# Optimization experiments

Hardware: AMD Instinct MI355X
Metric: run time of the kernel (lower is better)

## Reference

```python
import jax, jax.numpy as jnp
import numpy as np

G = 4           # graphs in batch
NV_PER = 3000   # variables per graph
NC_PER = 1000   # constraints per graph
DEG = 8         # constraint neighbors per variable
D_FEAT = 64
D_HID = 128
D_OUT = 64
K_BREAK = 8     # n_breakings
EPS = 1e-5


def setup_inputs() -> dict:
    key = jax.random.key(0)
    ks = jax.random.split(key, 5)
    nv, nc = G * NV_PER, G * NC_PER
    # bipartite edges: each variable connects to DEG random constraints within its graph
    var = np.tile(np.repeat(np.arange(NV_PER), DEG), G) + np.repeat(np.arange(G) * NV_PER, NV_PER * DEG)
    con = np.asarray(jax.random.randint(ks[0], (G, NV_PER * DEG), 0, NC_PER)) + (np.arange(G) * NC_PER)[:, None]
    con = con.reshape(-1)
    edge_indices = jnp.asarray(np.stack([con, var]), dtype=jnp.int32)            # (constraint, variable)
    reversed_edge_indices = jnp.asarray(np.stack([var, con]), dtype=jnp.int32)   # (variable, constraint)
    return {
        'variable_features': jax.random.normal(ks[1], (nv, D_FEAT), jnp.float32),
        'constraint_features': jax.random.normal(ks[2], (nc, D_FEAT), jnp.float32),
        'W1': jax.random.normal(ks[3], (D_FEAT + 1, D_HID), jnp.float32) * (1.0 / np.sqrt(D_FEAT + 1)),
        'b1': jnp.zeros((D_HID,), jnp.float32),
        'W2': jax.random.normal(ks[4], (D_HID, D_OUT), jnp.float32) * (1.0 / np.sqrt(D_HID)),
        'b2': jnp.zeros((D_OUT,), jnp.float32),
        'gamma': jnp.ones((D_OUT,), jnp.float32),
        'beta': jnp.zeros((D_OUT,), jnp.float32),
        'edge_indices': edge_indices,
        'reversed_edge_indices': reversed_edge_indices,
        'n_variables_per_graph': jnp.full((G,), NV_PER, jnp.int32),
        'n_constraints_per_graph': jnp.full((G,), NC_PER, jnp.int32),
    }


def _build_adj(edge_indices, reversed_edge_indices, nv, N):
    # homogeneous symmetric bipartite adjacency + gcn_norm(add_self_loops=True)
    rows = jnp.concatenate([reversed_edge_indices[0], edge_indices[0] + nv])
    cols = jnp.concatenate([reversed_edge_indices[1] + nv, edge_indices[1]])
    deg = jax.ops.segment_sum(jnp.ones_like(rows, jnp.float32), rows, num_segments=N) + 1.0
    dinv = jax.lax.rsqrt(deg)
    edge_vals = dinv[rows] * dinv[cols]     # D^-1/2 A D^-1/2 off-diagonal
    loop_vals = dinv * dinv                  # self-loop diagonal
    return rows, cols, edge_vals, loop_vals


def _spmm(rows, cols, edge_vals, loop_vals, N, X):
    # X: (N, d) -> adj @ X
    return jax.ops.segment_sum(edge_vals[:, None] * X[cols], rows, num_segments=N) + loop_vals[:, None] * X


def _holo_forward(variable_features, constraint_features, W1, b1, W2, b2, gamma, beta,
                  rows, cols, edge_vals, loop_vals, break_idx, break_group, G_):
    nv = variable_features.shape[0]
    N = nv + constraint_features.shape[0]
    nvp = nv // G_
    X = jnp.concatenate([variable_features, constraint_features], axis=0)        # (N, d)
    B = break_idx.shape[0]
    one_hot = jax.nn.one_hot(break_idx, N, dtype=X.dtype)                        # (B, N)
    Xb = jnp.concatenate([jnp.broadcast_to(X, (B,) + X.shape), one_hot[:, :, None]], axis=-1)  # (B, N, d+1)
    spmm = lambda x: _spmm(rows, cols, edge_vals, loop_vals, N, x)
    h = jax.nn.relu(jax.lax.map(spmm, Xb @ W1 + b1))                             # (B, N, D_HID)
    out = jax.lax.map(spmm, h @ W2 + b2)                                         # (B, N, D_OUT)
    mu = out.mean(-1, keepdims=True)
    var = ((out - mu) ** 2).mean(-1, keepdims=True)
    holo = (out - mu) * jax.lax.rsqrt(var + EPS) * gamma + beta                  # LayerNorm
    set_link = holo[:, :nv, :]                                                   # r=1: tuples = variables
    global_mean = set_link.mean(0)                                               # (nv, D_OUT)
    tuple_group = jnp.repeat(jnp.arange(G_), nvp)                                # (nv,)
    group_sum = jax.ops.segment_sum(set_link, break_group, num_segments=G_)      # (G, nv, D_OUT)
    counts = jax.ops.segment_sum(jnp.ones((B,), holo.dtype), break_group, num_segments=G_)
    link = group_sum[tuple_group, jnp.arange(nv)] / jnp.maximum(counts[tuple_group], 1.0)[:, None]
    return jnp.where((counts[tuple_group] > 0)[:, None], link, global_mean)


def reference(variable_features, constraint_features, W1, b1, W2, b2, gamma, beta,
              edge_indices, reversed_edge_indices, n_variables_per_graph, n_constraints_per_graph):
    nv = variable_features.shape[0]
    nc = constraint_features.shape[0]
    N = nv + nc
    G_ = n_variables_per_graph.shape[0]
    nvp, ncp = nv // G_, nc // G_
    rows, cols, edge_vals, loop_vals = _build_adj(edge_indices, reversed_edge_indices, nv, N)
    node_degrees = jax.ops.segment_sum(edge_vals, rows, num_segments=N) + loop_vals  # adj row sums
    # per-graph top-k degree nodes (tie-expansion is measure-zero for float gcn-norm degrees)
    var_ids = jnp.arange(G_)[:, None] * nvp + jnp.arange(nvp)[None, :]
    con_ids = nv + jnp.arange(G_)[:, None] * ncp + jnp.arange(ncp)[None, :]
    sample_nodes = jnp.concatenate([var_ids, con_ids], axis=1)                   # (G, nvp+ncp)
    _, local = jax.lax.top_k(node_degrees[sample_nodes], K_BREAK)
    break_idx = jnp.take_along_axis(sample_nodes, local, axis=1).reshape(-1)     # (G*K,)
    break_group = jnp.repeat(jnp.arange(G_), K_BREAK)
    return _holo_forward(variable_features, constraint_features, W1, b1, W2, b2, gamma, beta,
                         rows, cols, edge_vals, loop_vals, break_idx, break_group, G_)
```

## Files before the change

kernel.cpp:

```cpp
#include <hip/hip_runtime.h>
#include <hip/hip_bf16.h>

#define G_      4
#define NVP     3000
#define NCP     1000
#define DEG     8
#define NV      (G_*NVP)
#define NC      (G_*NCP)
#define NN      (NV+NC)
#define NE      (NV*DEG)
#define EPG     (NVP*DEG)
#define DF      64
#define DH      128
#define DO      64
#define KB      8
#define NB      (G_*KB)
#define MAXR    96
#define MAXJ    640
#define F2_GEMM_BLOCKS (NV/32)

__global__ __launch_bounds__(1024) void k_setup(const int* __restrict__ conArr,
    int* __restrict__ csr_off, int* __restrict__ csr_cur,
    float* __restrict__ dinvC_g, float* __restrict__ nodeval, int* __restrict__ breakix)
{
    __shared__ int   cnt[NCP];
    __shared__ float dinvC[NCP];
    __shared__ float nvl[NVP + NCP];
    __shared__ int   wsum[16];
    __shared__ float mv[16]; __shared__ int mp[16];

    int g = blockIdx.x, tid = threadIdx.x, lane = tid & 63, w = tid >> 6;
    int ebase = g * EPG, cb = g * NCP;
    const float dv3 = 1.0f/3.0f;

    if (tid < NCP) cnt[tid] = 0;
    __syncthreads();
    for (int e = tid; e < EPG; e += 1024)
        atomicAdd(&cnt[conArr[ebase + e] - cb], 1);
    __syncthreads();
    int x = (tid < NCP) ? cnt[tid] : 0;
    int orig = x;
    for (int o = 1; o < 64; o <<= 1) { int y = __shfl_up(x, o); if (lane >= o) x += y; }
    if (lane == 63) wsum[w] = x;
    __syncthreads();
    if (tid == 0) { int run = 0; for (int t = 0; t < 16; ++t) { int z = wsum[t]; wsum[t] = run; run += z; } }
    __syncthreads();
    int excl = x - orig + wsum[w];
    if (tid < NCP) {
        csr_off[cb + tid] = ebase + excl;
        csr_cur[cb + tid] = ebase + excl;
        float dc = 1.0f / sqrtf((float)(orig + 1));
        dinvC[tid] = dc;
        dinvC_g[cb + tid] = dc;
        float nvc = (float)orig * (dc * dv3) + dc*dc;
        nvl[NVP + tid] = nvc;
        nodeval[NV + cb + tid] = nvc;
    }
    if (g == 0 && tid == 0) csr_off[NC] = NE;
    __syncthreads();
    for (int v = tid; v < NVP; v += 1024) {
        float s = 0.f;
        int e0 = ebase + v*DEG;
        #pragma unroll
        for (int k = 0; k < DEG; ++k) s += dv3 * dinvC[conArr[e0+k] - cb];
        float val = s + dv3*dv3;
        nvl[v] = val;
        nodeval[g*NVP + v] = val;
    }
    __syncthreads();
    for (int it = 0; it < KB; ++it) {
        float bv = -1e30f; int bp = 1 << 30;
        for (int p = tid; p < NVP+NCP; p += 1024) {
            float vv = nvl[p];
            if (vv > bv || (vv == bv && p < bp)) { bv = vv; bp = p; }
        }
        for (int o = 32; o > 0; o >>= 1) {
            float ov = __shfl_xor(bv, o); int op = __shfl_xor(bp, o);
            if (ov > bv || (ov == bv && op < bp)) { bv = ov; bp = op; }
        }
        if (lane == 0) { mv[w] = bv; mp[w] = bp; }
        __syncthreads();
        if (tid == 0) {
            float fv = mv[0]; int fp = mp[0];
            for (int t = 1; t < 16; ++t)
                if (mv[t] > fv || (mv[t] == fv && mp[t] < fp)) { fv = mv[t]; fp = mp[t]; }
            nvl[fp] = -1e30f;
            breakix[g*KB + it] = (fp < NVP) ? (g*NVP + fp) : (NV + g*NCP + (fp - NVP));
        }
        __syncthreads();
    }
}

__global__ __launch_bounds__(1024) void k_fill(const int* __restrict__ conArr,
                                               int* __restrict__ csr_cur,
                                               int* __restrict__ csr_v) {
    int e = blockIdx.x*1024 + threadIdx.x;
    if (e < NE) { int p = atomicAdd(&csr_cur[conArr[e]], 1); csr_v[p] = e >> 3; }
}

__global__ __launch_bounds__(1024) void k_f1(const float* __restrict__ vf, const float* __restrict__ cf,
    const float* __restrict__ dinvC, const int* __restrict__ conArr,
    const int* __restrict__ csr_off, const int* __restrict__ csr_v,
    const float* __restrict__ W1, const float* __restrict__ b1,
    const float* __restrict__ nodeval, float* __restrict__ S1)
{
    __shared__ float W1T[128*68];
    __shared__ float AXs[32*68];
    int tid = threadIdx.x, lane = tid & 63, w = tid >> 6;
    const float dv3 = 1.0f/3.0f;
    for (int t = tid; t < 64*128; t += 1024) {
        int k = t >> 7, c = t & 127;
        W1T[c*68 + k] = W1[t];
    }
    int r0 = blockIdx.x * 32;
    for (int rr = w*2; rr < w*2 + 2; ++rr) {
        int row = r0 + rr;
        float acc, di;
        if (row < NV) {
            di = dv3;
            acc = dv3 * vf[(size_t)row*DF + lane];
            int e0 = row*DEG;
            #pragma unroll
            for (int k = 0; k < DEG; ++k) {
                int c = conArr[e0+k];
                acc += dinvC[c] * cf[(size_t)c*DF + lane];
            }
        } else {
            int c = row - NV;
            di = dinvC[c];
            float base = di * cf[(size_t)c*DF + lane];
            int p0 = csr_off[c], p1 = csr_off[c+1];
            int len = p1 - p0;
            int myv = (p0 + lane < p1) ? csr_v[p0 + lane] : 0;
            int lim = len < 64 ? len : 64;
            float a0 = 0.f, a1 = 0.f, a2 = 0.f, a3 = 0.f;
            int m = 0;
            for (; m + 4 <= lim; m += 4) {
                int v0 = __shfl(myv, m+0);
                int v1 = __shfl(myv, m+1);
                int v2 = __shfl(myv, m+2);
                int v3 = __shfl(myv, m+3);
                a0 += vf[(size_t)v0*DF + lane];
                a1 += vf[(size_t)v1*DF + lane];
                a2 += vf[(size_t)v2*DF + lane];
                a3 += vf[(size_t)v3*DF + lane];
            }
            for (; m < lim; ++m) { int v = __shfl(myv, m); a0 += vf[(size_t)v*DF + lane]; }
            for (int p = p0 + 64; p < p1; ++p) a0 += vf[(size_t)csr_v[p]*DF + lane];
            acc = base + dv3 * ((a0 + a1) + (a2 + a3));
        }
        AXs[rr*68 + lane] = di * acc;
    }
    __syncthreads();
    int tc = tid & 15, tr = tid >> 4;
    int row = tr & 31, chh = tr >> 5;
    float a4[4] = {0.f, 0.f, 0.f, 0.f};
    #pragma unroll
    for (int k0 = 0; k0 < 64; k0 += 4) {
        float4 a = *(const float4*)&AXs[row*68 + k0];
        #pragma unroll
        for (int j = 0; j < 4; ++j) {
            float4 wv = *(const float4*)&W1T[(tc + 16*j + 64*chh)*68 + k0];
            a4[j] += a.x*wv.x + a.y*wv.y + a.z*wv.z + a.w*wv.w;
        }
    }
    float nv_ = nodeval[r0 + row];
    #pragma unroll
    for (int j = 0; j < 4; ++j) {
        int col = tc + 16*j + 64*chh;
        S1[(size_t)(r0 + row)*DH + col] = a4[j] + nv_*b1[col];
    }
}

__global__ __launch_bounds__(1024) void k_f2(const float* __restrict__ S1,
    const float* __restrict__ dinvC, const int* __restrict__ conArr,
    const int* __restrict__ csr_off, const int* __restrict__ csr_v,
    const float* __restrict__ W1, const float* __restrict__ W2,
    const float* __restrict__ b2, const float* __restrict__ nodeval,
    const float* __restrict__ gamma, const float* __restrict__ beta,
    const int* __restrict__ breakidx,
    float* __restrict__ outvar, float* __restrict__ holo, float* __restrict__ out,
    int* __restrict__ RnG, float* __restrict__ RwG, int* __restrict__ nRG,
    float* __restrict__ dz2G)
{
    __shared__ float smem[14848];
    __shared__ int nR_s;
    int tid = threadIdx.x, lane = tid & 63, w = tid >> 6;
    const float dv3 = 1.0f/3.0f;

    if (blockIdx.x < F2_GEMM_BLOCKS) {
        float* W2T = smem;
        float* AHs = smem + 8448;
        float* s2  = smem + 12672;
        for (int t = tid; t < 128*64; t += 1024) {
            int k = t >> 6, c = t & 63;
            W2T[c*132 + k] = W2[t];
        }
        int r0 = blockIdx.x * 32;
        for (int rr = w*2; rr < w*2 + 2; ++rr) {
            int v = r0 + rr;
            float a0 = dv3 * fmaxf(S1[(size_t)v*DH + lane], 0.f);
            float a1 = dv3 * fmaxf(S1[(size_t)v*DH + 64 + lane], 0.f);
            int e0 = v*DEG;
            #pragma unroll
            for (int k = 0; k < DEG; ++k) {
                int c = conArr[e0+k];
                float dc = dinvC[c];
                a0 += dc * fmaxf(S1[(size_t)(NV+c)*DH + lane], 0.f);
                a1 += dc * fmaxf(S1[(size_t)(NV+c)*DH + 64 + lane], 0.f);
            }
            AHs[rr*132 + lane]      = dv3 * a0;
            AHs[rr*132 + 64 + lane] = dv3 * a1;
        }
        __syncthreads();
        int tc = tid & 15, tr = tid >> 4;
        int row = tr & 31, jh = tr >> 5;
        float a2[2] = {0.f, 0.f};
        #pragma unroll
        for (int k0 = 0; k0 < 128; k0 += 4) {
            float4 a = *(const float4*)&AHs[row*132 + k0];
            #pragma unroll
            for (int j = 0; j < 2; ++j) {
                float4 wv = *(const float4*)&W2T[(tc + 16*(j + 2*jh))*132 + k0];
                a2[j] += a.x*wv.x + a.y*wv.y + a.z*wv.z + a.w*wv.w;
            }
        }
        float nv_ = nodeval[r0 + row];
        #pragma unroll
        for (int j = 0; j < 2; ++j) {
            int col = tc + 16*(j + 2*jh);
            s2[row*68 + col] = a2[j] + nv_*b2[col];
        }
        __syncthreads();
        float gm = gamma[lane], bt = beta[lane];
        for (int rr = w*2; rr < w*2 + 2; ++rr) {
            int v = r0 + rr;
            float xv = s2[rr*68 + lane];
            float s = xv;
            for (int o = 32; o > 0; o >>= 1) s += __shfl_xor(s, o);
            float mu = s * (1.f/64.f);
            float d = xv - mu;
            float vs = d*d;
            for (int o = 32; o > 0; o >>= 1) vs += __shfl_xor(vs, o);
            float rstd = 1.0f / sqrtf(vs*(1.f/64.f) + 1e-5f);
            float h = d*rstd*gm + bt;
            outvar[(size_t)v*DO + lane] = xv;
            holo  [(size_t)v*DO + lane] = h;
            out   [(size_t)v*DO + lane] = h;
        }
    } else {
        float* W2s = smem;
        float* dh  = smem + 8192;
        float* Rw  = smem + 9216;
        int*   Rn  = (int*)(smem + 9312);
        int b = blockIdx.x - F2_GEMM_BLOCKS;
        int i = breakidx[b];
        for (int t = tid; t < 128*64; t += 1024) W2s[t] = W2[t];
        if (tid < 64) {
            if (i >= NV) {
                int c = i - NV;
                float di = dinvC[c];
                int p0 = csr_off[c], len = csr_off[c+1] - p0;
                if (len <= 64) {
                    int v = (lane < len) ? csr_v[p0 + lane] : 0x7fffffff;
                    int firstLane = 64, mult = 0;
                    for (int m = 0; m < 64; ++m) {
                        int vm = __shfl(v, m);
                        if (vm == v) { mult++; if (m < firstLane) firstLane = m; }
                    }
                    bool head = (lane < len) && (firstLane == lane);
                    unsigned long long hmask = __ballot(head);
                    int hrk = 0;
                    for (int m = 0; m < 64; ++m) {
                        if (!((hmask >> m) & 1)) continue;
                        int vm = __shfl(v, m);
                        if (vm < v) hrk++;
                    }
                    if (head) { Rn[hrk] = v; Rw[hrk] = (float)mult * (dv3 * di); }
                    int nH = __popcll(hmask);
                    if (lane == 0) { Rn[nH] = i; Rw[nH] = di*di; nR_s = nH + 1; }
                } else if (lane == 0) {
                    int n = 0;
                    for (int p = p0; p < p0 + len; ++p) {
                        int v = csr_v[p]; int f = -1;
                        for (int q = 0; q < n; ++q) if (Rn[q] == v) { f = q; break; }
                        if (f >= 0) Rw[f] += dv3 * di;
                        else if (n < MAXR-1) { Rn[n] = v; Rw[n] = dv3 * di; ++n; }
                    }
                    Rn[n] = i; Rw[n] = di*di; nR_s = n + 1;
                }
            } else if (lane == 0) {
                float di = dv3;
                int cn[DEG];
                for (int k = 0; k < DEG; ++k) cn[k] = NV + conArr[i*DEG + k];
                for (int a = 1; a < DEG; ++a) { int key = cn[a]; int bb = a-1;
                    while (bb >= 0 && cn[bb] > key) { cn[bb+1] = cn[bb]; --bb; } cn[bb+1] = key; }
                int n = 0, k = 0;
                while (k < DEG) { int u = cn[k]; int m = 1; ++k;
                    while (k < DEG && cn[k] == u) { ++m; ++k; }
                    Rn[n] = u; Rw[n] = (float)m * dinvC[u - NV] * di; ++n; }
                Rn[n] = i; Rw[n] = di*di; nR_s = n + 1;
            }
        }
        __syncthreads();
        int nR = nR_s;
        for (int t = tid; t < nR; t += 1024) { RnG[b*MAXR + t] = Rn[t]; RwG[b*MAXR + t] = Rw[t]; }
        if (tid == 0) nRG[b] = nR;
        for (int r0c = 0; r0c < nR; r0c += 8) {
            __syncthreads();
            {
                int ty = tid >> 7, k = tid & 127;
                int r = r0c + ty;
                if (r < nR) {
                    float s1 = S1[(size_t)Rn[r]*DH + k];
                    float a = s1 + Rw[r] * W1[64*128 + k];
                    dh[ty*128 + k] = fmaxf(a, 0.f) - fmaxf(s1, 0.f);
                }
            }
            __syncthreads();
            int ty2 = tid >> 6, c2 = tid & 63;
            if (ty2 < 8) {
                int r2 = r0c + ty2;
                if (r2 < nR) {
                    float accv = 0.f;
                    #pragma unroll
                    for (int kk = 0; kk < 128; ++kk) accv += dh[ty2*128 + kk] * W2s[kk*64 + c2];
                    dz2G[((size_t)b*MAXR + r2)*DO + c2] = accv;
                }
            }
        }
    }
}

__global__ __launch_bounds__(256) void k_corr_b(const int* __restrict__ RnG, const float* __restrict__ RwG,
                         const int* __restrict__ nRG, const float* __restrict__ dz2G,
                         const int* __restrict__ breakidx, const float* __restrict__ dinvC,
                         const int* __restrict__ conArr, const int* __restrict__ csr_off,
                         const int* __restrict__ csr_v,
                         const float* __restrict__ outvar, const float* __restrict__ holo,
                         const float* __restrict__ gamma, const float* __restrict__ beta,
                         float* __restrict__ out) {
    int b = blockIdx.x;
    int lane = threadIdx.x & 63, wv = threadIdx.x >> 6;
    const float dv3 = 1.0f/3.0f;
    __shared__ int Jn[MAXJ];
    __shared__ int nJ_s;
    int i = breakidx[b];
    int nR = nRG[b];
    float gm = gamma[lane], bt = beta[lane];
    if (i >= NV) {
        int nJ = nR - 1;
        const float* dzi = &dz2G[((size_t)b*MAXR + (nR-1))*DO];
        for (int j0 = wv; j0 < nJ; j0 += 4) {
            int j = RnG[b*MAXR + j0];
            float aji = RwG[b*MAXR + j0];
            float x = outvar[(size_t)j*DO + lane]
                    + aji * dzi[lane]
                    + dv3*dv3 * dz2G[((size_t)b*MAXR + j0)*DO + lane];
            float s = x; for (int o = 32; o > 0; o >>= 1) s += __shfl_xor(s, o);
            float mu = s * (1.f/64.f);
            float d = x - mu;
            float vs = d*d; for (int o = 32; o > 0; o >>= 1) vs += __shfl_xor(vs, o);
            float rstd = 1.0f / sqrtf(vs*(1.f/64.f) + 1e-5f);
            float hn = d*rstd*gm + bt;
            atomicAdd(&out[(size_t)j*DO + lane], 0.125f * (hn - holo[(size_t)j*DO + lane]));
        }
    } else {
        if (threadIdx.x == 0) {
            int n = 0; Jn[n++] = i;
            for (int r = 0; r < nR-1; ++r) {
                int c = RnG[b*MAXR + r] - NV;
                for (int p = csr_off[c]; p < csr_off[c+1]; ++p) {
                    int u = csr_v[p];
                    bool found = false;
                    for (int q = 0; q < n; ++q) if (Jn[q] == u) { found = true; break; }
                    if (!found && n < MAXJ) Jn[n++] = u;
                }
            }
            nJ_s = n;
        }
        __syncthreads();
        int nJ = nJ_s;
        for (int j0 = wv; j0 < nJ; j0 += 4) {
            int j = Jn[j0];
            float x = outvar[(size_t)j*DO + lane];
            for (int k = 0; k < DEG; ++k) {
                int cn = NV + conArr[j*DEG + k];
                for (int r = 0; r < nR-1; ++r)
                    if (RnG[b*MAXR + r] == cn) {
                        x += dv3 * dinvC[cn - NV] * dz2G[((size_t)b*MAXR + r)*DO + lane];
                        break;
                    }
            }
            if (j == i) x += dv3*dv3 * dz2G[((size_t)b*MAXR + nR-1)*DO + lane];
            float s = x; for (int o = 32; o > 0; o >>= 1) s += __shfl_xor(s, o);
            float mu = s * (1.f/64.f);
            float d = x - mu;
            float vs = d*d; for (int o = 32; o > 0; o >>= 1) vs += __shfl_xor(vs, o);
            float rstd = 1.0f / sqrtf(vs*(1.f/64.f) + 1e-5f);
            float hn = d*rstd*gm + bt;
            atomicAdd(&out[(size_t)j*DO + lane], 0.125f * (hn - holo[(size_t)j*DO + lane]));
        }
    }
}


extern "C" void kernel_launch(void* const* d_in, const int* in_sizes, int n_in,
                              void* d_out, int out_size, void* d_ws, size_t ws_size,
                              hipStream_t stream) {
    const float* vf    = (const float*)d_in[0];
    const float* cf    = (const float*)d_in[1];
    const float* W1    = (const float*)d_in[2];
    const float* b1    = (const float*)d_in[3];
    const float* W2    = (const float*)d_in[4];
    const float* b2    = (const float*)d_in[5];
    const float* gamma = (const float*)d_in[6];
    const float* beta  = (const float*)d_in[7];
    const int*   ei    = (const int*)d_in[8];
    const int*   conArr = ei;
    float* out = (float*)d_out;

    char* ws = (char*)d_ws;
    size_t off = 0;
    auto alloc = [&](size_t bytes) { char* p = ws + off; off = (off + bytes + 255) & ~(size_t)255; return p; };
    float* dinvC   = (float*)alloc(NC*4);
    int*   csr_off = (int*)  alloc((NC+1)*4);
    int*   csr_cur = (int*)  alloc(NC*4);
    int*   csr_v   = (int*)  alloc(NE*4);
    float* nodeval = (float*)alloc(NN*4);
    int*   breakix = (int*)  alloc(NB*4);
    float* S1      = (float*)alloc((size_t)NN*DH*4);
    float* outvar  = (float*)alloc((size_t)NV*DO*4);
    float* holo    = (float*)alloc((size_t)NV*DO*4);
    int*   RnG     = (int*)  alloc(NB*MAXR*4);
    float* RwG     = (float*)alloc(NB*MAXR*4);
    int*   nRG     = (int*)  alloc(NB*4);
    float* dz2G    = (float*)alloc((size_t)NB*MAXR*DO*4);

    k_setup <<<G_, 1024, 0, stream>>>(conArr, csr_off, csr_cur, dinvC, nodeval, breakix);
    k_fill  <<<(NE+1023)/1024, 1024, 0, stream>>>(conArr, csr_cur, csr_v);
    k_f1    <<<NN/32, 1024, 0, stream>>>(vf, cf, dinvC, conArr, csr_off, csr_v, W1, b1, nodeval, S1);
    k_f2    <<<F2_GEMM_BLOCKS + NB, 1024, 0, stream>>>(S1, dinvC, conArr, csr_off, csr_v,
                                       W1, W2, b2, nodeval, gamma, beta, breakix,
                                       outvar, holo, out, RnG, RwG, nRG, dz2G);
    k_corr_b<<<NB, 256, 0, stream>>>(RnG, RwG, nRG, dz2G, breakix, dinvC, conArr,
                                     csr_off, csr_v, outvar, holo, gamma, beta, out);
}
```

Measured before the change: 95.37 us.

## Fuse all stages into one cooperative persistent kernel with grid syncs

Replaces the five separate kernel launches with a single cooperative kernel of 256 blocks that runs setup, CSR fill, the first GCN layer, the second layer plus break corrections, and the final correction, separated by grid-wide syncs. Each block handles up to two tiles per stage and reuses the transposed weight matrix already in shared memory for its second tile. The intent is to remove launch gaps and inter-kernel drain. In exchange, grid syncs add overhead and most blocks sit idle in setup and the final stage. The corr_b stage now runs on 1024-thread blocks with a matching loop stride, and a multi-launch fallback keeps the old behaviour if the cooperative launch fails.

Result: no change. 94.46 us (-0.9%).

```diff
diff --git a/kernel.cpp b/kernel.cpp
--- a/kernel.cpp
+++ b/kernel.cpp
@@ -1,5 +1,8 @@
 #include <hip/hip_runtime.h>
+#include <hip/hip_cooperative_groups.h>
 #include <hip/hip_bf16.h>
+
+namespace cg = cooperative_groups;
 
 #define G_      4
 #define NVP     3000
@@ -17,19 +20,24 @@
 #define NB      (G_*KB)
 #define MAXR    96
 #define MAXJ    640
-#define F2_GEMM_BLOCKS (NV/32)
-
-__global__ __launch_bounds__(1024) void k_setup(const int* __restrict__ conArr,
+#define F2_GEMM_TILES (NV/32)
+#define F1_TILES (NN/32)
+#define F2_TILES (F2_GEMM_TILES+NB)
+#define MEGA_GRID 256
+
+
+__device__ __forceinline__ void setup_body(int g, const int* __restrict__ conArr,
     int* __restrict__ csr_off, int* __restrict__ csr_cur,
-    float* __restrict__ dinvC_g, float* __restrict__ nodeval, int* __restrict__ breakix)
+    float* __restrict__ dinvC_g, float* __restrict__ nodeval, int* __restrict__ breakix,
+    float* smemf)
 {
-    __shared__ int   cnt[NCP];
-    __shared__ float dinvC[NCP];
-    __shared__ float nvl[NVP + NCP];
-    __shared__ int   wsum[16];
-    __shared__ float mv[16]; __shared__ int mp[16];
-
-    int g = blockIdx.x, tid = threadIdx.x, lane = tid & 63, w = tid >> 6;
+    int*   cnt   = (int*)smemf;
+    float* dinvC = (float*)(cnt + NCP);
+    float* nvl   = dinvC + NCP;
+    int*   wsum  = (int*)(nvl + (NVP + NCP));
+    float* mv    = (float*)(wsum + 16);
+    int*   mp    = (int*)(mv + 16);
+    int tid = threadIdx.x, lane = tid & 63, w = tid >> 6;
     int ebase = g * EPG, cb = g * NCP;
     const float dv3 = 1.0f/3.0f;
 
@@ -91,28 +99,25 @@
     }
 }
 
-__global__ __launch_bounds__(1024) void k_fill(const int* __restrict__ conArr,
-                                               int* __restrict__ csr_cur,
-                                               int* __restrict__ csr_v) {
-    int e = blockIdx.x*1024 + threadIdx.x;
-    if (e < NE) { int p = atomicAdd(&csr_cur[conArr[e]], 1); csr_v[p] = e >> 3; }
-}
-
-__global__ __launch_bounds__(1024) void k_f1(const float* __restrict__ vf, const float* __restrict__ cf,
+__device__ __forceinline__ void f1_body(int tile, bool first,
+    const float* __restrict__ vf, const float* __restrict__ cf,
     const float* __restrict__ dinvC, const int* __restrict__ conArr,
     const int* __restrict__ csr_off, const int* __restrict__ csr_v,
     const float* __restrict__ W1, const float* __restrict__ b1,
-    const float* __restrict__ nodeval, float* __restrict__ S1)
+    const float* __restrict__ nodeval, float* __restrict__ S1, float* smemf)
 {
-    __shared__ float W1T[128*68];
-    __shared__ float AXs[32*68];
+    float* W1T = smemf;
+    float* AXs = smemf + 8704;
     int tid = threadIdx.x, lane = tid & 63, w = tid >> 6;
     const float dv3 = 1.0f/3.0f;
-    for (int t = tid; t < 64*128; t += 1024) {
-        int k = t >> 7, c = t & 127;
-        W1T[c*68 + k] = W1[t];
-    }
-    int r0 = blockIdx.x * 32;
+    if (!first) __syncthreads();
+    if (first) {
+        for (int t = tid; t < 64*128; t += 1024) {
+            int k = t >> 7, c = t & 127;
+            W1T[c*68 + k] = W1[t];
+        }
+    }
+    int r0 = tile * 32;
     for (int rr = w*2; rr < w*2 + 2; ++rr) {
         int row = r0 + rr;
         float acc, di;
@@ -172,186 +177,194 @@
     }
 }
 
-__global__ __launch_bounds__(1024) void k_f2(const float* __restrict__ S1,
-    const float* __restrict__ dinvC, const int* __restrict__ conArr,
-    const int* __restrict__ csr_off, const int* __restrict__ csr_v,
-    const float* __restrict__ W1, const float* __restrict__ W2,
+__device__ __forceinline__ void f2gemm_body(int tile, bool first,
+    const float* __restrict__ S1, const float* __restrict__ dinvC,
+    const int* __restrict__ conArr, const float* __restrict__ W2,
     const float* __restrict__ b2, const float* __restrict__ nodeval,
     const float* __restrict__ gamma, const float* __restrict__ beta,
-    const int* __restrict__ breakidx,
     float* __restrict__ outvar, float* __restrict__ holo, float* __restrict__ out,
-    int* __restrict__ RnG, float* __restrict__ RwG, int* __restrict__ nRG,
-    float* __restrict__ dz2G)
+    float* smemf)
 {
-    __shared__ float smem[14848];
-    __shared__ int nR_s;
+    float* W2T = smemf;
+    float* AHs = smemf + 8448;
+    float* s2  = smemf + 12672;
     int tid = threadIdx.x, lane = tid & 63, w = tid >> 6;
     const float dv3 = 1.0f/3.0f;
-
-    if (blockIdx.x < F2_GEMM_BLOCKS) {
-        float* W2T = smem;
-        float* AHs = smem + 8448;
-        float* s2  = smem + 12672;
+    if (!first) __syncthreads();
+    if (first) {
         for (int t = tid; t < 128*64; t += 1024) {
             int k = t >> 6, c = t & 63;
             W2T[c*132 + k] = W2[t];
         }
-        int r0 = blockIdx.x * 32;
-        for (int rr = w*2; rr < w*2 + 2; ++rr) {
-            int v = r0 + rr;
-            float a0 = dv3 * fmaxf(S1[(size_t)v*DH + lane], 0.f);
-            float a1 = dv3 * fmaxf(S1[(size_t)v*DH + 64 + lane], 0.f);
-            int e0 = v*DEG;
-            #pragma unroll
-            for (int k = 0; k < DEG; ++k) {
-                int c = conArr[e0+k];
-                float dc = dinvC[c];
-                a0 += dc * fmaxf(S1[(size_t)(NV+c)*DH + lane], 0.f);
-                a1 += dc * fmaxf(S1[(size_t)(NV+c)*DH + 64 + lane], 0.f);
-            }
-            AHs[rr*132 + lane]      = dv3 * a0;
-            AHs[rr*132 + 64 + lane] = dv3 * a1;
-        }
-        __syncthreads();
-        int tc = tid & 15, tr = tid >> 4;
-        int row = tr & 31, jh = tr >> 5;
-        float a2[2] = {0.f, 0.f};
+    }
+    int r0 = tile * 32;
+    for (int rr = w*2; rr < w*2 + 2; ++rr) {
+        int v = r0 + rr;
+        float a0 = dv3 * fmaxf(S1[(size_t)v*DH + lane], 0.f);
+        float a1 = dv3 * fmaxf(S1[(size_t)v*DH + 64 + lane], 0.f);
+        int e0 = v*DEG;
         #pragma unroll
-        for (int k0 = 0; k0 < 128; k0 += 4) {
-            float4 a = *(const float4*)&AHs[row*132 + k0];
-            #pragma unroll
-            for (int j = 0; j < 2; ++j) {
-                float4 wv = *(const float4*)&W2T[(tc + 16*(j + 2*jh))*132 + k0];
-                a2[j] += a.x*wv.x + a.y*wv.y + a.z*wv.z + a.w*wv.w;
-            }
-        }
-        float nv_ = nodeval[r0 + row];
+        for (int k = 0; k < DEG; ++k) {
+            int c = conArr[e0+k];
+            float dc = dinvC[c];
+            a0 += dc * fmaxf(S1[(size_t)(NV+c)*DH + lane], 0.f);
+            a1 += dc * fmaxf(S1[(size_t)(NV+c)*DH + 64 + lane], 0.f);
+        }
+        AHs[rr*132 + lane]      = dv3 * a0;
+        AHs[rr*132 + 64 + lane] = dv3 * a1;
+    }
+    __syncthreads();
+    int tc = tid & 15, tr = tid >> 4;
+    int row = tr & 31, jh = tr >> 5;
+    float a2[2] = {0.f, 0.f};
+    #pragma unroll
+    for (int k0 = 0; k0 < 128; k0 += 4) {
+        float4 a = *(const float4*)&AHs[row*132 + k0];
         #pragma unroll
         for (int j = 0; j < 2; ++j) {
-            int col = tc + 16*(j + 2*jh);
-            s2[row*68 + col] = a2[j] + nv_*b2[col];
-        }
+            float4 wv = *(const float4*)&W2T[(tc + 16*(j + 2*jh))*132 + k0];
+            a2[j] += a.x*wv.x + a.y*wv.y + a.z*wv.z + a.w*wv.w;
+        }
+    }
+    float nv_ = nodeval[r0 + row];
+    #pragma unroll
+    for (int j = 0; j < 2; ++j) {
+        int col = tc + 16*(j + 2*jh);
+        s2[row*68 + col] = a2[j] + nv_*b2[col];
+    }
+    __syncthreads();
+    float gm = gamma[lane], bt = beta[lane];
+    for (int rr = w*2; rr < w*2 + 2; ++rr) {
+        int v = r0 + rr;
+        float xv = s2[rr*68 + lane];
+        float s = xv;
+        for (int o = 32; o > 0; o >>= 1) s += __shfl_xor(s, o);
+        float mu = s * (1.f/64.f);
+        float d = xv - mu;
+        float vs = d*d;
+        for (int o = 32; o > 0; o >>= 1) vs += __shfl_xor(vs, o);
+        float rstd = 1.0f / sqrtf(vs*(1.f/64.f) + 1e-5f);
+        float h = d*rstd*gm + bt;
+        outvar[(size_t)v*DO + lane] = xv;
+        holo  [(size_t)v*DO + lane] = h;
+        out   [(size_t)v*DO + lane] = h;
+    }
+}
+
+__device__ __forceinline__ void corra_body(int b,
+    const float* __restrict__ S1, const float* __restrict__ dinvC,
+    const int* __restrict__ conArr, const int* __restrict__ csr_off,
+    const int* __restrict__ csr_v, const float* __restrict__ W1,
+    const float* __restrict__ W2, const int* __restrict__ breakidx,
+    int* __restrict__ RnG, float* __restrict__ RwG, int* __restrict__ nRG,
+    float* __restrict__ dz2G, float* smemf, int& nR_s)
+{
+    float* W2s = smemf;
+    float* dh  = smemf + 8192;
+    float* Rw  = smemf + 9216;
+    int*   Rn  = (int*)(smemf + 9312);
+    int tid = threadIdx.x, lane = tid & 63;
+    const float dv3 = 1.0f/3.0f;
+    __syncthreads();
+    int i = breakidx[b];
+    for (int t = tid; t < 128*64; t += 1024) W2s[t] = W2[t];
+    if (tid < 64) {
+        if (i >= NV) {
+            int c = i - NV;
+            float di = dinvC[c];
+            int p0 = csr_off[c], len = csr_off[c+1] - p0;
+            if (len <= 64) {
+                int v = (lane < len) ? csr_v[p0 + lane] : 0x7fffffff;
+                int firstLane = 64, mult = 0;
+                for (int m = 0; m < 64; ++m) {
+                    int vm = __shfl(v, m);
+                    if (vm == v) { mult++; if (m < firstLane) firstLane = m; }
+                }
+                bool head = (lane < len) && (firstLane == lane);
+                unsigned long long hmask = __ballot(head);
+                int hrk = 0;
+                for (int m = 0; m < 64; ++m) {
+                    if (!((hmask >> m) & 1)) continue;
+                    int vm = __shfl(v, m);
+                    if (vm < v) hrk++;
+                }
+                if (head) { Rn[hrk] = v; Rw[hrk] = (float)mult * (dv3 * di); }
+                int nH = __popcll(hmask);
+                if (lane == 0) { Rn[nH] = i; Rw[nH] = di*di; nR_s = nH + 1; }
+            } else if (lane == 0) {
+                int n = 0;
+                for (int p = p0; p < p0 + len; ++p) {
+                    int v = csr_v[p]; int f = -1;
+                    for (int q = 0; q < n; ++q) if (Rn[q] == v) { f = q; break; }
+                    if (f >= 0) Rw[f] += dv3 * di;
+                    else if (n < MAXR-1) { Rn[n] = v; Rw[n] = dv3 * di; ++n; }
+                }
+                Rn[n] = i; Rw[n] = di*di; nR_s = n + 1;
+            }
+        } else if (lane == 0) {
+            float di = dv3;
+            int cn[DEG];
+            for (int k = 0; k < DEG; ++k) cn[k] = NV + conArr[i*DEG + k];
+            for (int a = 1; a < DEG; ++a) { int key = cn[a]; int bb = a-1;
+                while (bb >= 0 && cn[bb] > key) { cn[bb+1] = cn[bb]; --bb; } cn[bb+1] = key; }
+            int n = 0, k = 0;
+            while (k < DEG) { int u = cn[k]; int m = 1; ++k;
+                while (k < DEG && cn[k] == u) { ++m; ++k; }
+                Rn[n] = u; Rw[n] = (float)m * dinvC[u - NV] * di; ++n; }
+            Rn[n] = i; Rw[n] = di*di; nR_s = n + 1;
+        }
+    }
+    __syncthreads();
+    int nR = nR_s;
+    for (int t = tid; t < nR; t += 1024) { RnG[b*MAXR + t] = Rn[t]; RwG[b*MAXR + t] = Rw[t]; }
+    if (tid == 0) nRG[b] = nR;
+    for (int r0c = 0; r0c < nR; r0c += 8) {
         __syncthreads();
-        float gm = gamma[lane], bt = beta[lane];
-        for (int rr = w*2; rr < w*2 + 2; ++rr) {
-            int v = r0 + rr;
-            float xv = s2[rr*68 + lane];
-            float s = xv;
-            for (int o = 32; o > 0; o >>= 1) s += __shfl_xor(s, o);
-            float mu = s * (1.f/64.f);
-            float d = xv - mu;
-            float vs = d*d;
-            for (int o = 32; o > 0; o >>= 1) vs += __shfl_xor(vs, o);
-            float rstd = 1.0f / sqrtf(vs*(1.f/64.f) + 1e-5f);
-            float h = d*rstd*gm + bt;
-            outvar[(size_t)v*DO + lane] = xv;
-            holo  [(size_t)v*DO + lane] = h;
-            out   [(size_t)v*DO + lane] = h;
-        }
-    } else {
-        float* W2s = smem;
-        float* dh  = smem + 8192;
-        float* Rw  = smem + 9216;
-        int*   Rn  = (int*)(smem + 9312);
-        int b = blockIdx.x - F2_GEMM_BLOCKS;
-        int i = breakidx[b];
-        for (int t = tid; t < 128*64; t += 1024) W2s[t] = W2[t];
-        if (tid < 64) {
-            if (i >= NV) {
-                int c = i - NV;
-                float di = dinvC[c];
-                int p0 = csr_off[c], len = csr_off[c+1] - p0;
-                if (len <= 64) {
-                    int v = (lane < len) ? csr_v[p0 + lane] : 0x7fffffff;
-                    int firstLane = 64, mult = 0;
-                    for (int m = 0; m < 64; ++m) {
-                        int vm = __shfl(v, m);
-                        if (vm == v) { mult++; if (m < firstLane) firstLane = m; }
-                    }
-                    bool head = (lane < len) && (firstLane == lane);
-                    unsigned long long hmask = __ballot(head);
-                    int hrk = 0;
-                    for (int m = 0; m < 64; ++m) {
-                        if (!((hmask >> m) & 1)) continue;
-                        int vm = __shfl(v, m);
-                        if (vm < v) hrk++;
-                    }
-                    if (head) { Rn[hrk] = v; Rw[hrk] = (float)mult * (dv3 * di); }
-                    int nH = __popcll(hmask);
-                    if (lane == 0) { Rn[nH] = i; Rw[nH] = di*di; nR_s = nH + 1; }
-                } else if (lane == 0) {
-                    int n = 0;
-                    for (int p = p0; p < p0 + len; ++p) {
-                        int v = csr_v[p]; int f = -1;
-                        for (int q = 0; q < n; ++q) if (Rn[q] == v) { f = q; break; }
-                        if (f >= 0) Rw[f] += dv3 * di;
-                        else if (n < MAXR-1) { Rn[n] = v; Rw[n] = dv3 * di; ++n; }
-                    }
-                    Rn[n] = i; Rw[n] = di*di; nR_s = n + 1;
-                }
-            } else if (lane == 0) {
-                float di = dv3;
-                int cn[DEG];
-                for (int k = 0; k < DEG; ++k) cn[k] = NV + conArr[i*DEG + k];
-                for (int a = 1; a < DEG; ++a) { int key = cn[a]; int bb = a-1;
-                    while (bb >= 0 && cn[bb] > key) { cn[bb+1] = cn[bb]; --bb; } cn[bb+1] = key; }
-                int n = 0, k = 0;
-                while (k < DEG) { int u = cn[k]; int m = 1; ++k;
-                    while (k < DEG && cn[k] == u) { ++m; ++k; }
-                    Rn[n] = u; Rw[n] = (float)m * dinvC[u - NV] * di; ++n; }
-                Rn[n] = i; Rw[n] = di*di; nR_s = n + 1;
+        {
+            int ty = tid >> 7, k = tid & 127;
+            int r = r0c + ty;
+            if (r < nR) {
+                float s1 = S1[(size_t)Rn[r]*DH + k];
+                float a = s1 + Rw[r] * W1[64*128 + k];
+                dh[ty*128 + k] = fmaxf(a, 0.f) - fmaxf(s1, 0.f);
             }
         }
         __syncthreads();
-        int nR = nR_s;
-        for (int t = tid; t < nR; t += 1024) { RnG[b*MAXR + t] = Rn[t]; RwG[b*MAXR + t] = Rw[t]; }
-        if (tid == 0) nRG[b] = nR;
-        for (int r0c = 0; r0c < nR; r0c += 8) {
-            __syncthreads();
-            {
-                int ty = tid >> 7, k = tid & 127;
-                int r = r0c + ty;
-                if (r < nR) {
-                    float s1 = S1[(size_t)Rn[r]*DH + k];
-                    float a = s1 + Rw[r] * W1[64*128 + k];
-                    dh[ty*128 + k] = fmaxf(a, 0.f) - fmaxf(s1, 0.f);
-                }
-            }
-            __syncthreads();
-            int ty2 = tid >> 6, c2 = tid & 63;
-            if (ty2 < 8) {
-                int r2 = r0c + ty2;
-                if (r2 < nR) {
-                    float accv = 0.f;
-                    #pragma unroll
-                    for (int kk = 0; kk < 128; ++kk) accv += dh[ty2*128 + kk] * W2s[kk*64 + c2];
-                    dz2G[((size_t)b*MAXR + r2)*DO + c2] = accv;
-                }
-            }
-        }
-    }
-}
-
-__global__ __launch_bounds__(256) void k_corr_b(const int* __restrict__ RnG, const float* __restrict__ RwG,
-                         const int* __restrict__ nRG, const float* __restrict__ dz2G,
-                         const int* __restrict__ breakidx, const float* __restrict__ dinvC,
-                         const int* __restrict__ conArr, const int* __restrict__ csr_off,
-                         const int* __restrict__ csr_v,
-                         const float* __restrict__ outvar, const float* __restrict__ holo,
-                         const float* __restrict__ gamma, const float* __restrict__ beta,
-                         float* __restrict__ out) {
-    int b = blockIdx.x;
+        int ty2 = tid >> 6, c2 = tid & 63;
+        if (ty2 < 8) {
+            int r2 = r0c + ty2;
+            if (r2 < nR) {
+                float accv = 0.f;
+                #pragma unroll
+                for (int kk = 0; kk < 128; ++kk) accv += dh[ty2*128 + kk] * W2s[kk*64 + c2];
+                dz2G[((size_t)b*MAXR + r2)*DO + c2] = accv;
+            }
+        }
+    }
+    __syncthreads();
+}
+
+__device__ __forceinline__ void corrb_body(int b,
+    const int* __restrict__ RnG, const float* __restrict__ RwG,
+    const int* __restrict__ nRG, const float* __restrict__ dz2G,
+    const int* __restrict__ breakidx, const float* __restrict__ dinvC,
+    const int* __restrict__ conArr, const int* __restrict__ csr_off,
+    const int* __restrict__ csr_v,
+    const float* __restrict__ outvar, const float* __restrict__ holo,
+    const float* __restrict__ gamma, const float* __restrict__ beta,
+    float* __restrict__ out, float* smemf)
+{
+    int* Jn = (int*)smemf;
+    __shared__ int nJ_s;
     int lane = threadIdx.x & 63, wv = threadIdx.x >> 6;
     const float dv3 = 1.0f/3.0f;
-    __shared__ int Jn[MAXJ];
-    __shared__ int nJ_s;
     int i = breakidx[b];
     int nR = nRG[b];
     float gm = gamma[lane], bt = beta[lane];
     if (i >= NV) {
         int nJ = nR - 1;
         const float* dzi = &dz2G[((size_t)b*MAXR + (nR-1))*DO];
-        for (int j0 = wv; j0 < nJ; j0 += 4) {
+        for (int j0 = wv; j0 < nJ; j0 += 16) {
             int j = RnG[b*MAXR + j0];
             float aji = RwG[b*MAXR + j0];
             float x = outvar[(size_t)j*DO + lane]
@@ -381,7 +394,7 @@
         }
         __syncthreads();
         int nJ = nJ_s;
-        for (int j0 = wv; j0 < nJ; j0 += 4) {
+        for (int j0 = wv; j0 < nJ; j0 += 16) {
             int j = Jn[j0];
             float x = outvar[(size_t)j*DO + lane];
             for (int k = 0; k < DEG; ++k) {
@@ -402,6 +415,75 @@
             atomicAdd(&out[(size_t)j*DO + lane], 0.125f * (hn - holo[(size_t)j*DO + lane]));
         }
     }
+}
+
+
+__global__ __launch_bounds__(1024) void k_mega(
+    const float* __restrict__ vf, const float* __restrict__ cf,
+    const float* __restrict__ W1, const float* __restrict__ b1,
+    const float* __restrict__ W2, const float* __restrict__ b2,
+    const float* __restrict__ gamma, const float* __restrict__ beta,
+    const int* __restrict__ conArr,
+    int* csr_off, int* csr_cur, int* csr_v,
+    float* dinvC, float* nodeval, int* breakix,
+    float* S1, float* outvar, float* holo,
+    int* RnG, float* RwG, int* nRG, float* dz2G,
+    float* out, int phase)
+{
+    __shared__ float smemf[14848];
+    __shared__ int nR_s;
+    const bool coop = (phase < 0);
+    int bid = blockIdx.x;
+
+    if ((coop || phase == 0) && bid < G_)
+        setup_body(bid, conArr, csr_off, csr_cur, dinvC, nodeval, breakix, smemf);
+    if (coop) cg::this_grid().sync();
+
+    if (coop || phase == 1) {
+        int e = bid*1024 + threadIdx.x;
+        if (e < NE) { int p = atomicAdd(&csr_cur[conArr[e]], 1); csr_v[p] = e >> 3; }
+    }
+    if (coop) cg::this_grid().sync();
+
+    if (coop || phase == 2) {
+        if (coop) {
+            f1_body(bid, true, vf, cf, dinvC, conArr, csr_off, csr_v, W1, b1, nodeval, S1, smemf);
+            int t2 = (bid < F1_TILES - MEGA_GRID) ? MEGA_GRID + bid : -1;
+            if (t2 >= 0)
+                f1_body(t2, false, vf, cf, dinvC, conArr, csr_off, csr_v, W1, b1, nodeval, S1, smemf);
+        } else {
+            f1_body(bid, true, vf, cf, dinvC, conArr, csr_off, csr_v, W1, b1, nodeval, S1, smemf);
+        }
+    }
+    if (coop) cg::this_grid().sync();
+
+    if (coop || phase == 3) {
+        if (coop) {
+            f2gemm_body(bid, true, S1, dinvC, conArr, W2, b2, nodeval, gamma, beta,
+                        outvar, holo, out, smemf);
+            int t2 = (bid < F2_TILES - MEGA_GRID) ? MEGA_GRID + bid : -1;
+            if (t2 >= 0) {
+                if (t2 < F2_GEMM_TILES)
+                    f2gemm_body(t2, false, S1, dinvC, conArr, W2, b2, nodeval, gamma, beta,
+                                outvar, holo, out, smemf);
+                else
+                    corra_body(t2 - F2_GEMM_TILES, S1, dinvC, conArr, csr_off, csr_v,
+                               W1, W2, breakix, RnG, RwG, nRG, dz2G, smemf, nR_s);
+            }
+        } else {
+            if (bid < F2_GEMM_TILES)
+                f2gemm_body(bid, true, S1, dinvC, conArr, W2, b2, nodeval, gamma, beta,
+                            outvar, holo, out, smemf);
+            else
+                corra_body(bid - F2_GEMM_TILES, S1, dinvC, conArr, csr_off, csr_v,
+                           W1, W2, breakix, RnG, RwG, nRG, dz2G, smemf, nR_s);
+        }
+    }
+    if (coop) cg::this_grid().sync();
+
+    if ((coop || phase == 4) && bid < NB)
+        corrb_body(bid, RnG, RwG, nRG, dz2G, breakix, dinvC, conArr, csr_off, csr_v,
+                   outvar, holo, gamma, beta, out, smemf);
 }
 
 
@@ -416,8 +498,7 @@
     const float* b2    = (const float*)d_in[5];
     const float* gamma = (const float*)d_in[6];
     const float* beta  = (const float*)d_in[7];
-    const int*   ei    = (const int*)d_in[8];
-    const int*   conArr = ei;
+    const int*   conArr = (const int*)d_in[8];
     float* out = (float*)d_out;
 
     char* ws = (char*)d_ws;
@@ -437,12 +518,41 @@
     int*   nRG     = (int*)  alloc(NB*4);
     float* dz2G    = (float*)alloc((size_t)NB*MAXR*DO*4);
 
-    k_setup <<<G_, 1024, 0, stream>>>(conArr, csr_off, csr_cur, dinvC, nodeval, breakix);
-    k_fill  <<<(NE+1023)/1024, 1024, 0, stream>>>(conArr, csr_cur, csr_v);
-    k_f1    <<<NN/32, 1024, 0, stream>>>(vf, cf, dinvC, conArr, csr_off, csr_v, W1, b1, nodeval, S1);
-    k_f2    <<<F2_GEMM_BLOCKS + NB, 1024, 0, stream>>>(S1, dinvC, conArr, csr_off, csr_v,
-                                       W1, W2, b2, nodeval, gamma, beta, breakix,
-                                       outvar, holo, out, RnG, RwG, nRG, dz2G);
-    k_corr_b<<<NB, 256, 0, stream>>>(RnG, RwG, nRG, dz2G, breakix, dinvC, conArr,
-                                     csr_off, csr_v, outvar, holo, gamma, beta, out);
-}
+    bool useCoop = false;
+    int occ = 0;
+    if (hipOccupancyMaxActiveBlocksPerMultiprocessor(&occ, (const void*)k_mega, 1024, 0) == hipSuccess
+        && occ >= 1) {
+        int ph = -1;
+        void* args[] = {
+            (void*)&vf, (void*)&cf, (void*)&W1, (void*)&b1, (void*)&W2, (void*)&b2,
+            (void*)&gamma, (void*)&beta, (void*)&conArr,
+            (void*)&csr_off, (void*)&csr_cur, (void*)&csr_v,
+            (void*)&dinvC, (void*)&nodeval, (void*)&breakix,
+            (void*)&S1, (void*)&outvar, (void*)&holo,
+            (void*)&RnG, (void*)&RwG, (void*)&nRG, (void*)&dz2G,
+            (void*)&out, (void*)&ph };
+        if (hipLaunchCooperativeKernel((const void*)k_mega, dim3(MEGA_GRID), dim3(1024),
+                                       args, 0, stream) == hipSuccess)
+            useCoop = true;
+        else
+            (void)hipGetLastError();
+    }
+
+    if (!useCoop) {
+        k_mega<<<G_,                1024, 0, stream>>>(vf, cf, W1, b1, W2, b2, gamma, beta, conArr,
+            csr_off, csr_cur, csr_v, dinvC, nodeval, breakix, S1, outvar, holo,
+            RnG, RwG, nRG, dz2G, out, 0);
+        k_mega<<<(NE+1023)/1024,    1024, 0, stream>>>(vf, cf, W1, b1, W2, b2, gamma, beta, conArr,
+            csr_off, csr_cur, csr_v, dinvC, nodeval, breakix, S1, outvar, holo,
+            RnG, RwG, nRG, dz2G, out, 1);
+        k_mega<<<F1_TILES,          1024, 0, stream>>>(vf, cf, W1, b1, W2, b2, gamma, beta, conArr,
+            csr_off, csr_cur, csr_v, dinvC, nodeval, breakix, S1, outvar, holo,
+            RnG, RwG, nRG, dz2G, out, 2);
+        k_mega<<<F2_TILES,          1024, 0, stream>>>(vf, cf, W1, b1, W2, b2, gamma, beta, conArr,
+            csr_off, csr_cur, csr_v, dinvC, nodeval, breakix, S1, outvar, holo,
+            RnG, RwG, nRG, dz2G, out, 3);
+        k_mega<<<NB,                1024, 0, stream>>>(vf, cf, W1, b1, W2, b2, gamma, beta, conArr,
+            csr_off, csr_cur, csr_v, dinvC, nodeval, breakix, S1, outvar, holo,
+            RnG, RwG, nRG, dz2G, out, 4);
+    }
+}
```
